# Optimization experiments

Measured on AMD Instinct MI355X. Metric: run time of the kernel, lower is better.

## Reference

```python
import jax, jax.numpy as jnp
from jax import lax
import numpy as np

D_MODEL = 1024
D_STATE = 64
D_CONV = 4
EXPAND = 2
HEADDIM = 64
D_INNER = EXPAND * D_MODEL          # 2048
NHEADS = D_INNER // HEADDIM         # 32
CHUNK = 64
CONV_DIM = D_INNER + 2 * D_STATE    # 2176
D_IN_PROJ = 2 * D_INNER + 2 * D_STATE + NHEADS  # 4256
B_SZ = 4
SEQLEN = 2048
EPS = 1e-5


def _silu(x):
    return x * jax.nn.sigmoid(x)


def _segsum(x):
    # x: [..., T]; returns [..., T, T] with [i,j] = sum_{j<k<=i} x[k], -inf above diag
    T = x.shape[-1]
    xe = jnp.broadcast_to(x[..., None], x.shape + (T,))
    strict_lower = jnp.tril(jnp.ones((T, T), bool), -1)
    xe = jnp.where(strict_lower, xe, 0.0)
    s = jnp.cumsum(xe, axis=-2)
    lower = jnp.tril(jnp.ones((T, T), bool), 0)
    return jnp.where(lower, s, -jnp.inf)


def setup_inputs() -> dict:
    key = jax.random.key(0)
    ks = jax.random.split(key, 5)
    u = jax.random.normal(ks[0], (B_SZ, SEQLEN, D_MODEL), jnp.float32)
    W_in = jax.random.normal(ks[1], (D_IN_PROJ, D_MODEL), jnp.float32) * 0.02
    conv_w = jax.random.normal(ks[2], (CONV_DIM, 1, D_CONV), jnp.float32) * 0.2  # depthwise kernel
    conv_b = jnp.zeros((CONV_DIM,), jnp.float32)
    dt_bias = jax.random.uniform(ks[3], (NHEADS,), jnp.float32, -1.0, 1.0)
    A_log = jnp.log(jnp.linspace(1.0, float(NHEADS), NHEADS)).astype(jnp.float32)
    D = jnp.ones((NHEADS,), jnp.float32)
    norm_w = jnp.ones((D_INNER,), jnp.float32)
    W_out = jax.random.normal(ks[4], (D_MODEL, D_INNER), jnp.float32) * 0.02
    return dict(u=u, W_in=W_in, conv_w=conv_w, conv_b=conv_b, dt_bias=dt_bias,
                A_log=A_log, D=D, norm_w=norm_w, W_out=W_out)


def reference(u, W_in, conv_w, conv_b, dt_bias, A_log, D, norm_w, W_out):
    b, s, _ = u.shape
    A = -jnp.exp(A_log)                                   # [H]
    zxbcdt = u @ W_in.T                                   # [b,s,D_IN_PROJ]
    z = zxbcdt[..., :D_INNER]
    xBC = zxbcdt[..., D_INNER:D_INNER + CONV_DIM]
    dt = jax.nn.softplus(zxbcdt[..., D_INNER + CONV_DIM:] + dt_bias)  # [b,s,H]

    # causal depthwise conv1d (left pad d_conv-1 == torch pad-both + slice[:s])
    xc = lax.conv_general_dilated(
        xBC.transpose(0, 2, 1), conv_w, window_strides=(1,),
        padding=[(D_CONV - 1, 0)], feature_group_count=CONV_DIM,
        dimension_numbers=('NCH', 'OIH', 'NCH'))
    xBC = _silu(xc.transpose(0, 2, 1) + conv_b)           # [b,s,CONV_DIM]

    x = xBC[..., :D_INNER].reshape(b, s, NHEADS, HEADDIM)
    Bm = xBC[..., D_INNER:D_INNER + D_STATE]              # [b,s,N]
    Cm = xBC[..., D_INNER + D_STATE:]                     # [b,s,N]

    # SSD chunked scan
    nch = s // CHUNK
    xs = (x * dt[..., None]).reshape(b, nch, CHUNK, NHEADS, HEADDIM)
    Ad = (A * dt).reshape(b, nch, CHUNK, NHEADS)
    Br = Bm.reshape(b, nch, CHUNK, D_STATE)
    Cr = Cm.reshape(b, nch, CHUNK, D_STATE)
    A_ch = Ad.transpose(0, 1, 3, 2)                       # [b,c,h,l]
    A_cum = jnp.cumsum(A_ch, axis=-1)
    L = jnp.exp(_segsum(A_ch))                            # [b,c,h,l,l]
    Y_diag = jnp.einsum('bcln,bcsn,bchls,bcshp->bclhp', Cr, Br, L, xs)
    decay_states = jnp.exp(A_cum[..., -1:] - A_cum)       # [b,c,h,l]
    states = jnp.einsum('bchl,bcln,bclhp->bchpn', decay_states, Br, xs)
    init = jnp.zeros((b, 1, NHEADS, HEADDIM, D_STATE), xs.dtype)
    states = jnp.concatenate([init, states], axis=1)      # [b,c+1,h,p,n]
    total_decay = jnp.pad(A_cum[..., -1].transpose(0, 2, 1), ((0, 0), (0, 0), (1, 0)))
    decay_chunk = jnp.exp(_segsum(total_decay))           # [b,h,c+1,c+1]
    new_states = jnp.einsum('bhzc,bchpn->bzhpn', decay_chunk, states)
    states = new_states[:, :-1]                           # [b,c,h,p,n]
    state_decay_out = jnp.exp(A_cum)
    Y_off = jnp.einsum('bcln,bchpn,bchl->bclhp', Cr, states, state_decay_out)
    y = (Y_diag + Y_off).reshape(b, s, NHEADS, HEADDIM)

    y = y + x * D[:, None]
    y = y.reshape(b, s, D_INNER)
    # gated RMSNorm
    y = y * _silu(z)
    y = y * lax.rsqrt(jnp.mean(y * y, axis=-1, keepdims=True) + EPS) * norm_w
    return y @ W_out.T
```

## Files before the change

### kernel.cpp

```cpp
#include <hip/hip_runtime.h>
#include <hip/hip_bf16.h>

#define BSZ 4
#define SEQ 2048
#define DMODEL 1024
#define DINNER 2048
#define DSTATE 64
#define NH 32
#define HD 64
#define CKL 64
#define NCH 32
#define CONVD 2176
#define DPROJ 4256
#define N1 4224
#define MTOT 8192
#define YSTR 72
#define CVTB 6272

typedef __hip_bfloat16 bf16;
typedef __attribute__((ext_vector_type(8))) short short8;
typedef __attribute__((ext_vector_type(4))) short short4_;
typedef __attribute__((ext_vector_type(4))) float f32x4;

__device__ __forceinline__ float sigmoidf_(float x) { return 1.0f / (1.0f + __expf(-x)); }
__device__ __forceinline__ float bits2f(short s) { return __uint_as_float(((unsigned)(unsigned short)s) << 16); }
__device__ __forceinline__ short f2bits(float f) {
    bf16 h = __float2bfloat16(f);
    return *reinterpret_cast<short*>(&h);
}

__device__ __forceinline__ void gl_lds16(const bf16* g, bf16* l) {
    __builtin_amdgcn_global_load_lds((const __attribute__((address_space(1))) void*)g,
                                     (__attribute__((address_space(3))) void*)l, 16, 0, 0);
}

__device__ __forceinline__ f32x4 MF(short8 a, short8 b, f32x4 c) {
    return __builtin_amdgcn_mfma_f32_16x16x32_bf16(a, b, c, 0, 0, 0);
}

template<int N> __device__ __forceinline__ void vmw() {
    if constexpr (N == 0)      asm volatile("s_waitcnt vmcnt(0)" ::: "memory");
    else if constexpr (N == 3) asm volatile("s_waitcnt vmcnt(3)" ::: "memory");
    else if constexpr (N == 6) asm volatile("s_waitcnt vmcnt(6)" ::: "memory");
    else                       asm volatile("s_waitcnt vmcnt(15)" ::: "memory");
}

__device__ __forceinline__ void swzx(int& bx, int& by) {
    int nx = gridDim.x;
    int nwg = nx * gridDim.y;
    int Lr = blockIdx.y * nx + blockIdx.x;
    int L = (Lr & 7) * (nwg >> 3) + (Lr >> 3);
    int GSZ = nx * 8;
    int g = L / GSZ, r = L - g * GSZ;
    bx = r % nx;
    by = g * 8 + r / nx;
}

__global__ __launch_bounds__(256) void k_pre2(const float* __restrict__ u, const float* __restrict__ W_in,
                                              const float* __restrict__ dt_bias,
                                              const float* __restrict__ W_out, const float* __restrict__ nw,
                                              bf16* __restrict__ u_b, float* __restrict__ dtt,
                                              bf16* __restrict__ win_b, bf16* __restrict__ wout_b) {
    __shared__ __align__(16) float us[8 * DMODEL];
    const int tid = threadIdx.x;
    if (blockIdx.x < CVTB) {
        int g = (blockIdx.x * 256 + tid) * 4;
        if (g < N1 * DMODEL) {
            f32x4 f = *(const f32x4*)&W_in[g];
            short4_ o;
#pragma unroll
            for (int j = 0; j < 4; j++) o[j] = f2bits(f[j]);
            *(short4_*)&win_b[g] = o;
        } else if (g < N1 * DMODEL + DMODEL * DINNER) {
            int g2 = g - N1 * DMODEL;
            f32x4 f = *(const f32x4*)&W_out[g2];
            f32x4 w = *(const f32x4*)&nw[g2 & (DINNER - 1)];
            short4_ o;
#pragma unroll
            for (int j = 0; j < 4; j++) o[j] = f2bits(f[j] * w[j]);
            *(short4_*)&wout_b[g2] = o;
        }
        return;
    }
    const int t0 = (blockIdx.x - CVTB) * 8;
    const float* ur = u + (size_t)t0 * DMODEL;
    bf16* ub = u_b + (size_t)t0 * DMODEL;
#pragma unroll
    for (int i = 0; i < 8; i++) {
        int idx = (i * 256 + tid) * 4;
        f32x4 v = *(const f32x4*)&ur[idx];
        *(f32x4*)&us[idx] = v;
        short4_ o;
#pragma unroll
        for (int j = 0; j < 4; j++) o[j] = f2bits(v[j]);
        *(short4_*)&ub[idx] = o;
    }
    __syncthreads();
    const int h = tid >> 3, sub = tid & 7;
    const float* wr = W_in + (size_t)(DPROJ - NH + h) * DMODEL;
    float s[8] = {};
    for (int k = sub * 4; k < DMODEL; k += 32) {
        f32x4 w4 = *(const f32x4*)&wr[k];
#pragma unroll
        for (int rr = 0; rr < 8; rr++) {
            f32x4 u4 = *(const f32x4*)&us[rr * DMODEL + k];
            s[rr] += u4[0] * w4[0] + u4[1] * w4[1] + u4[2] * w4[2] + u4[3] * w4[3];
        }
    }
#pragma unroll
    for (int rr = 0; rr < 8; rr++) {
        s[rr] += __shfl_down(s[rr], 4, 8);
        s[rr] += __shfl_down(s[rr], 2, 8);
        s[rr] += __shfl_down(s[rr], 1, 8);
    }
    if (sub == 0) {
        float bh = dt_bias[h];
#pragma unroll
        for (int rr = 0; rr < 8; rr++) {
            float x = s[rr] + bh;
            dtt[(size_t)h * MTOT + t0 + rr] = (x > 20.f) ? x : log1pf(__expf(x));
        }
    }
}

#define BARWAIT()                                           \
    __builtin_amdgcn_s_barrier();                           \
    asm volatile("s_waitcnt lgkmcnt(0)" ::: "memory");      \
    __builtin_amdgcn_sched_barrier(0);                      \
    __builtin_amdgcn_s_setprio(1)
#define ENDPH()                                             \
    __builtin_amdgcn_s_setprio(0);                          \
    __builtin_amdgcn_s_barrier()

__global__ __launch_bounds__(512, 2) void k_g1(const bf16* __restrict__ Ap,
                                               const bf16* __restrict__ Wp,
                                               bf16* __restrict__ Cp) {
    __shared__ __align__(16) short sA[2][16384];
    __shared__ __align__(16) short sB[2][12288];
    const int tid = threadIdx.x;
    const int lane = tid & 63, w = tid >> 6;
    const int wm = w >> 2, wn = w & 3;
    const int lr = lane & 15, lk = lane >> 4;
    int bx, by; swzx(bx, by);
    const int m0 = by * 256, n0 = bx * 192;
    const int ld = DMODEL;

    const int r8 = tid >> 3;
    const int c8 = ((tid & 7) ^ (r8 & 7)) * 8;
    const bf16* pA = Ap + (size_t)(m0 + r8) * ld + c8;
    const bf16* pB = Wp + (size_t)(n0 + r8) * ld + c8;

    auto stA = [&](int d, int t) {
#pragma unroll
        for (int h = 0; h < 2; h++)
#pragma unroll
            for (int q = 0; q < 2; q++)
                gl_lds16(pA + (size_t)(h * 128 + q * 64) * ld + t * 64,
                         (bf16*)&sA[d][h * 8192 + q * 4096 + tid * 8]);
    };
    auto stB = [&](int d, int u, int t) {
        gl_lds16(pB + (size_t)(u * 64) * ld + t * 64,
                 (bf16*)&sB[d][u * 4096 + tid * 8]);
    };

    const int c0 = (lk ^ (lr & 7)) * 8;
    const int c1 = ((lk + 4) ^ (lr & 7)) * 8;
    const int aR = (wm * 128 + lr) * 64;
    const int bR = (wn * 48 + lr) * 64;

    f32x4 acc[8][3];
#pragma unroll
    for (int i = 0; i < 8; i++)
#pragma unroll
        for (int j = 0; j < 3; j++) acc[i][j] = (f32x4){0.f, 0.f, 0.f, 0.f};
    short8 bfr[3][2], af[2][2];

#define RDA1(D, I)                                                   \
    af[0][0] = *(const short8*)&sA[D][aR + (I) * 1024 + c0];         \
    af[0][1] = *(const short8*)&sA[D][aR + (I) * 1024 + c1];         \
    af[1][0] = *(const short8*)&sA[D][aR + (I + 1) * 1024 + c0];     \
    af[1][1] = *(const short8*)&sA[D][aR + (I + 1) * 1024 + c1]
#define RDB1(D)                                                      \
    _Pragma("unroll")                                                \
    for (int jn = 0; jn < 3; ++jn) {                                 \
        bfr[jn][0] = *(const short8*)&sB[D][bR + jn * 1024 + c0];    \
        bfr[jn][1] = *(const short8*)&sB[D][bR + jn * 1024 + c1];    \
    }
#define MM1(I)                                                       \
    _Pragma("unroll")                                                \
    for (int hh = 0; hh < 2; ++hh) {                                 \
        _Pragma("unroll")                                            \
        for (int jn = 0; jn < 3; ++jn) {                             \
            acc[I][jn]     = MF(af[0][hh], bfr[jn][hh], acc[I][jn]); \
            acc[I + 1][jn] = MF(af[1][hh], bfr[jn][hh], acc[I + 1][jn]); \
        }                                                            \
    }

    stB(0, 0, 0); stB(0, 1, 0); stB(0, 2, 0); stA(0, 0);
    stB(1, 0, 1); stB(1, 1, 1); stB(1, 2, 1);
    vmw<3>();
    __builtin_amdgcn_s_barrier();

    for (int t0 = 0; t0 < 16; t0 += 2) {
        const int t1 = t0 + 1, t2 = t0 + 2, t3 = t0 + 3;
        const bool more = (t2 < 16);
        RDB1(0); RDA1(0, 0);
        stA(1, t1);
        BARWAIT(); MM1(0); ENDPH();
        RDA1(0, 2); if (more) stB(0, 0, t2);
        BARWAIT(); MM1(2); ENDPH();
        RDA1(0, 4); if (more) stB(0, 1, t2);
        BARWAIT(); MM1(4); ENDPH();
        RDA1(0, 6); if (more) stB(0, 2, t2);
        BARWAIT(); MM1(6);
        __builtin_amdgcn_s_setprio(0);
        if (more) vmw<3>(); else vmw<0>();
        __builtin_amdgcn_s_barrier();
        RDB1(1); RDA1(1, 0);
        if (more) stA(0, t2);
        BARWAIT(); MM1(0); ENDPH();
        RDA1(1, 2); if (more) stB(1, 0, t3);
        BARWAIT(); MM1(2); ENDPH();
        RDA1(1, 4); if (more) stB(1, 1, t3);
        BARWAIT(); MM1(4); ENDPH();
        RDA1(1, 6); if (more) stB(1, 2, t3);
        BARWAIT(); MM1(6);
        __builtin_amdgcn_s_setprio(0);
        if (more) vmw<3>();
        __builtin_amdgcn_s_barrier();
    }
#undef RDA1
#undef RDB1
#undef MM1

#pragma unroll
    for (int im = 0; im < 8; im++) {
        int row = m0 + wm * 128 + im * 16 + lk * 4;
#pragma unroll
        for (int jn = 0; jn < 3; jn++) {
            int col = n0 + wn * 48 + jn * 16 + lr;
            bf16* cp = Cp + (size_t)row * N1 + col;
#pragma unroll
            for (int rr = 0; rr < 4; rr++) cp[(size_t)rr * N1] = __float2bfloat16(acc[im][jn][rr]);
        }
    }
}

__global__ __launch_bounds__(512, 2) void k_g2(const bf16* __restrict__ Ap,
                                               const bf16* __restrict__ Wp,
                                               float* __restrict__ Cp) {
    __shared__ __align__(16) short sA[3][16384];
    __shared__ __align__(16) short sB[3][8192];
    __shared__ float rsrow[256];
    const int tid = threadIdx.x;
    const int lane = tid & 63, w = tid >> 6;
    const int wm = w >> 1, wn = w & 1;
    const int lr = lane & 15, lk = lane >> 4;
    int bx, by; swzx(bx, by);
    const int m0 = by * 256, n0 = bx * 128;
    const int lda = N1, ldb = DINNER;

    const int r8 = tid >> 3;
    const int c8 = ((tid & 7) ^ (r8 & 7)) * 8;
    const bf16* pA = Ap + (size_t)(m0 + r8) * lda + c8;
    const bf16* pB = Wp + (size_t)(n0 + r8) * ldb + c8;

    auto stA = [&](int d, int t) {
#pragma unroll
        for (int h = 0; h < 2; h++)
#pragma unroll
            for (int q = 0; q < 2; q++)
                gl_lds16(pA + (size_t)(h * 128 + q * 64) * lda + t * 64,
                         (bf16*)&sA[d][h * 8192 + q * 4096 + tid * 8]);
    };
    auto stB = [&](int d, int t) {
#pragma unroll
        for (int q = 0; q < 2; q++)
            gl_lds16(pB + (size_t)(q * 64) * ldb + t * 64,
                     (bf16*)&sB[d][q * 4096 + tid * 8]);
    };

    const int c0 = (lk ^ (lr & 7)) * 8;
    const int c1 = ((lk + 4) ^ (lr & 7)) * 8;
    const int aR = (wm * 64 + lr) * 64;
    const int bR = (wn * 64 + lr) * 64;

    f32x4 acc[4][4];
#pragma unroll
    for (int i = 0; i < 4; i++)
#pragma unroll
        for (int j = 0; j < 4; j++) acc[i][j] = (f32x4){0.f, 0.f, 0.f, 0.f};
    float ssq[4] = {0.f, 0.f, 0.f, 0.f};
    short8 bfr[4][2], af[2][2];

#define RDA2(D, I)                                                   \
    af[0][0] = *(const short8*)&sA[D][aR + (I) * 1024 + c0];         \
    af[0][1] = *(const short8*)&sA[D][aR + (I) * 1024 + c1];         \
    af[1][0] = *(const short8*)&sA[D][aR + (I + 1) * 1024 + c0];     \
    af[1][1] = *(const short8*)&sA[D][aR + (I + 1) * 1024 + c1]
#define RDB2(D)                                                      \
    _Pragma("unroll")                                                \
    for (int jn = 0; jn < 4; ++jn) {                                 \
        bfr[jn][0] = *(const short8*)&sB[D][bR + jn * 1024 + c0];    \
        bfr[jn][1] = *(const short8*)&sB[D][bR + jn * 1024 + c1];    \
    }
#define MM2(I)                                                       \
    _Pragma("unroll")                                                \
    for (int hh = 0; hh < 2; ++hh) {                                 \
        _Pragma("unroll")                                            \
        for (int jn = 0; jn < 4; ++jn) {                             \
            acc[I][jn]     = MF(af[0][hh], bfr[jn][hh], acc[I][jn]); \
            acc[I + 1][jn] = MF(af[1][hh], bfr[jn][hh], acc[I + 1][jn]); \
        }                                                            \
    }
#define SSQ2(I)                                                      \
    _Pragma("unroll")                                                \
    for (int hh = 0; hh < 2; ++hh)                                   \
        _Pragma("unroll")                                            \
        for (int e = 0; e < 8; ++e) {                                \
            float v0 = bits2f(af[0][hh][e]), v1 = bits2f(af[1][hh][e]); \
            ssq[I] += v0 * v0; ssq[I + 1] += v1 * v1;                \
        }

    stB(0, 0); stA(0, 0);
    stB(1, 1); stA(1, 1);
    vmw<6>();
    __builtin_amdgcn_s_barrier();

    int rb = 0, sb = 2;
    for (int t = 0; t < 32; ++t) {
        const bool more = (t + 2 < 32);
        RDB2(rb); RDA2(rb, 0);
        if (more) stB(sb, t + 2);
        BARWAIT(); MM2(0); SSQ2(0); ENDPH();
        RDA2(rb, 2);
        if (more) stA(sb, t + 2);
        BARWAIT(); MM2(2); SSQ2(2);
        __builtin_amdgcn_s_setprio(0);
        if (more) vmw<6>(); else if (t + 1 < 32) vmw<0>();
        __builtin_amdgcn_s_barrier();
        rb = (rb == 2) ? 0 : rb + 1;
        sb = (sb == 2) ? 0 : sb + 1;
    }
#undef RDA2
#undef RDB2
#undef MM2
#undef SSQ2

#pragma unroll
    for (int im = 0; im < 4; im++) {
        float s = ssq[im];
        s += __shfl_down(s, 32);
        s += __shfl_down(s, 16);
        if (lane < 16) rsrow[wm * 64 + im * 16 + lane] = rsqrtf(s * (1.0f / DINNER) + 1e-5f);
    }
    __syncthreads();
#pragma unroll
    for (int im = 0; im < 4; im++) {
        int rl = wm * 64 + im * 16 + lk * 4;
        int row = m0 + rl;
#pragma unroll
        for (int rr = 0; rr < 4; rr++) {
            float s = rsrow[rl + rr];
#pragma unroll
            for (int jn = 0; jn < 4; jn++) {
                int col = n0 + wn * 64 + jn * 16 + lr;
                Cp[(size_t)(row + rr) * DMODEL + col] = acc[im][jn][rr] * s;
            }
        }
    }
}

__global__ __launch_bounds__(256) void k_conv(const bf16* __restrict__ zx, const float* __restrict__ cw,
                                              const float* __restrict__ cb, bf16* __restrict__ xbc) {
    const int g = blockIdx.x * 256 + threadIdx.x;
    const int c0 = (g % 544) * 4;
    const int t0 = (g / 544) * 4;
    const int s0 = t0 & (SEQ - 1);
    const short* base = (const short*)(zx + (size_t)t0 * N1 + DINNER + c0);
    f32x4 w0 = *(const f32x4*)&cw[(c0 + 0) * 4];
    f32x4 w1 = *(const f32x4*)&cw[(c0 + 1) * 4];
    f32x4 w2 = *(const f32x4*)&cw[(c0 + 2) * 4];
    f32x4 w3 = *(const f32x4*)&cw[(c0 + 3) * 4];
    f32x4 bias = *(const f32x4*)&cb[c0];
    short4_ v[7];
#pragma unroll
    for (int o = 0; o < 7; o++) {
        if (s0 + o - 3 >= 0) v[o] = *(const short4_*)(base + (long)(o - 3) * N1);
        else v[o] = (short4_){0, 0, 0, 0};
    }
#pragma unroll
    for (int j = 0; j < 4; j++) {
        f32x4 a = bias;
#pragma unroll
        for (int k = 0; k < 4; k++) {
            short4_ x = v[j + k];
            a[0] += bits2f(x[0]) * w0[k];
            a[1] += bits2f(x[1]) * w1[k];
            a[2] += bits2f(x[2]) * w2[k];
            a[3] += bits2f(x[3]) * w3[k];
        }
        short4_ o_;
#pragma unroll
        for (int jj = 0; jj < 4; jj++) o_[jj] = f2bits(a[jj] * sigmoidf_(a[jj]));
        *(short4_*)((short*)xbc + (size_t)(t0 + j) * CONVD + c0) = o_;
    }
}

__global__ __launch_bounds__(256) void k_ssd(const bf16* __restrict__ xbc, const float* __restrict__ dtt,
                                             const float* __restrict__ A_log, const float* __restrict__ Dp,
                                             bf16* __restrict__ zx) {
    __shared__ __align__(16) short Ct[2][64 * YSTR];
    __shared__ __align__(16) short Bt[2][64 * YSTR];
    __shared__ __align__(16) short Bn[2][64 * YSTR];
    __shared__ __align__(16) short Xt[2][32 * YSTR];
    __shared__ __align__(16) short Sb[2][32 * YSTR];
    __shared__ __align__(16) short Gs[4 * 16 * YSTR];
    __shared__ __align__(16) float Sf[32 * 68];
    __shared__ __align__(16) float sdt2[2][64], sAc2[2][64], sf2[2][64];
    __shared__ float set2[2];

    const int ph = blockIdx.x, h = blockIdx.y, b = blockIdx.z;
    const int tid = threadIdx.x;
    const int lane = tid & 63, w = tid >> 6;
    const int lr = lane & 15, lk = lane >> 4;
    const float Ah = -__expf(A_log[h]);
    const float Dh = Dp[h];
    const int xcol = h * HD + ph * 32;

    const int lrow = tid >> 2, c0 = (tid & 3) * 16, px = (tid & 3) * 8;
    const int zl = 16 * w + (lane >> 2), zp = (lane & 3) * 8;

    short8 rC0, rC1, rB0, rB1, rX, rZ;
    float rdt;
    auto load_chunk = [&](int cc) {
        int rows0 = b * SEQ + cc * CKL;
        const short* rp = (const short*)(xbc + (size_t)(rows0 + lrow) * CONVD);
        rC0 = *(const short8*)&rp[DINNER + DSTATE + c0];
        rC1 = *(const short8*)&rp[DINNER + DSTATE + c0 + 8];
        rB0 = *(const short8*)&rp[DINNER + c0];
        rB1 = *(const short8*)&rp[DINNER + c0 + 8];
        rX  = *(const short8*)&rp[xcol + px];
        rZ  = *(const short8*)((const short*)zx + (size_t)(rows0 + zl) * N1 + xcol + zp);
        rdt = dtt[(size_t)h * MTOT + rows0 + lane];
    };
    auto scatter = [&](int buf) {
        *(short8*)&Ct[buf][lrow * YSTR + c0] = rC0;
        *(short8*)&Ct[buf][lrow * YSTR + c0 + 8] = rC1;
        *(short8*)&Bt[buf][lrow * YSTR + c0] = rB0;
        *(short8*)&Bt[buf][lrow * YSTR + c0 + 8] = rB1;
#pragma unroll
        for (int j = 0; j < 8; j++) {
            Bn[buf][(c0 + j) * YSTR + lrow] = rB0[j];
            Bn[buf][(c0 + 8 + j) * YSTR + lrow] = rB1[j];
            Xt[buf][(px + j) * YSTR + lrow] = rX[j];
        }
    };
    auto dtscan = [&](int buf) {
        if (tid < 64) {
            float dv = rdt;
            float v = Ah * dv;
#pragma unroll
            for (int d = 1; d < 64; d <<= 1) { float o = __shfl_up(v, d); if (tid >= d) v += o; }
            float tot = __shfl(v, 63);
            sdt2[buf][tid] = dv; sAc2[buf][tid] = v; sf2[buf][tid] = __expf(tot - v) * dv;
            if (tid == 63) set2[buf] = __expf(tot);
        }
    };

    for (int i = tid; i < 32 * 68; i += 256) Sf[i] = 0.f;
    for (int i = tid; i < 32 * YSTR; i += 256) Sb[0][i] = 0;
    load_chunk(0);
    scatter(0);
    dtscan(0);
    __syncthreads();

    for (int c = 0; c < NCH; c++) {
        const int par = c & 1, nb = par ^ 1;
        const int rows0 = b * SEQ + c * CKL;
        float etot = set2[par];
        short8 zcur = rZ;
        if (c + 1 < NCH) load_chunk(c + 1);

        short8 cf0 = *(const short8*)&Ct[par][(16 * w + lr) * YSTR + lk * 8];
        short8 cf1 = *(const short8*)&Ct[par][(16 * w + lr) * YSTR + 32 + lk * 8];
        f32x4 acc[2];
#pragma unroll
        for (int t = 0; t < 2; t++) {
            short8 s0 = *(const short8*)&Sb[par][(16 * t + lr) * YSTR + lk * 8];
            short8 s1 = *(const short8*)&Sb[par][(16 * t + lr) * YSTR + 32 + lk * 8];
            acc[t] = MF(cf0, s0, (f32x4){0.f, 0.f, 0.f, 0.f});
            acc[t] = MF(cf1, s1, acc[t]);
        }
        float sAcl[4], el[4];
#pragma unroll
        for (int rr = 0; rr < 4; rr++) { sAcl[rr] = sAc2[par][16 * w + lk * 4 + rr]; el[rr] = __expf(sAcl[rr]); }
#pragma unroll
        for (int t = 0; t < 2; t++)
#pragma unroll
            for (int rr = 0; rr < 4; rr++) acc[t][rr] *= el[rr];
        short* gw = Gs + w * 16 * YSTR;
#pragma unroll
        for (int t = 0; t < 4; t++) {
            short8 b0 = *(const short8*)&Bt[par][(16 * t + lr) * YSTR + lk * 8];
            short8 b1 = *(const short8*)&Bt[par][(16 * t + lr) * YSTR + 32 + lk * 8];
            f32x4 g = MF(cf0, b0, (f32x4){0.f, 0.f, 0.f, 0.f});
            g = MF(cf1, b1, g);
            int s = 16 * t + lr;
            float sAcs = sAc2[par][s], dts = sdt2[par][s];
#pragma unroll
            for (int rr = 0; rr < 4; rr++) {
                int l = 16 * w + lk * 4 + rr;
                float v = (s <= l) ? g[rr] * __expf(sAcl[rr] - sAcs) * dts : 0.f;
                gw[(lk * 4 + rr) * YSTR + s] = f2bits(v);
            }
        }
        short8 gf0 = *(const short8*)&gw[lr * YSTR + lk * 8];
        short8 gf1 = *(const short8*)&gw[lr * YSTR + 32 + lk * 8];
#pragma unroll
        for (int t = 0; t < 2; t++) {
            short8 x0 = *(const short8*)&Xt[par][(16 * t + lr) * YSTR + lk * 8];
            short8 x1 = *(const short8*)&Xt[par][(16 * t + lr) * YSTR + 32 + lk * 8];
            acc[t] = MF(gf0, x0, acc[t]);
            acc[t] = MF(gf1, x1, acc[t]);
        }
        {
            int pw = w & 1, nh2 = w >> 1;
            short8 xt0 = *(const short8*)&Xt[par][(16 * pw + lr) * YSTR + lk * 8];
            short8 xt1 = *(const short8*)&Xt[par][(16 * pw + lr) * YSTR + 32 + lk * 8];
            f32x4 sa0 = *(const f32x4*)&sf2[par][lk * 8];
            f32x4 sa1 = *(const f32x4*)&sf2[par][lk * 8 + 4];
            f32x4 sb0 = *(const f32x4*)&sf2[par][32 + lk * 8];
            f32x4 sb1 = *(const f32x4*)&sf2[par][32 + lk * 8 + 4];
            short8 xd0, xd1;
#pragma unroll
            for (int j = 0; j < 4; j++) {
                xd0[j]     = f2bits(bits2f(xt0[j])     * sa0[j]);
                xd0[4 + j] = f2bits(bits2f(xt0[4 + j]) * sa1[j]);
                xd1[j]     = f2bits(bits2f(xt1[j])     * sb0[j]);
                xd1[4 + j] = f2bits(bits2f(xt1[4 + j]) * sb1[j]);
            }
#pragma unroll
            for (int j = 0; j < 2; j++) {
                int nt = 2 * nh2 + j;
                short8 b0 = *(const short8*)&Bn[par][(16 * nt + lr) * YSTR + lk * 8];
                short8 b1 = *(const short8*)&Bn[par][(16 * nt + lr) * YSTR + 32 + lk * 8];
                f32x4 sacc = MF(xd0, b0, (f32x4){0.f, 0.f, 0.f, 0.f});
                sacc = MF(xd1, b1, sacc);
#pragma unroll
                for (int rr = 0; rr < 4; rr++) {
                    int n = 16 * nt + lr;
                    int p = 16 * pw + lk * 4 + rr;
                    float nv = Sf[p * 68 + n] * etot + sacc[rr];
                    Sf[p * 68 + n] = nv;
                    Sb[nb][p * YSTR + n] = f2bits(nv);
                }
            }
        }
#pragma unroll
        for (int t = 0; t < 2; t++) {
#pragma unroll
            for (int rr = 0; rr < 4; rr++) {
                int p = 16 * t + lr;
                int l = 16 * w + lk * 4 + rr;
                float y = acc[t][rr] + Dh * bits2f(Xt[par][p * YSTR + l]);
                Ct[par][l * YSTR + p] = f2bits(y);
            }
        }
        {
            short8 y8 = *(const short8*)&Ct[par][zl * YSTR + zp];
            short* zpp = (short*)zx + (size_t)(rows0 + zl) * N1 + xcol + zp;
            short8 o;
#pragma unroll
            for (int j = 0; j < 8; j++) {
                float z = bits2f(zcur[j]);
                o[j] = f2bits(bits2f(y8[j]) * (z * sigmoidf_(z)));
            }
            *(short8*)zpp = o;
        }
        if (c + 1 < NCH) {
            scatter(nb);
            dtscan(nb);
        }
        __syncthreads();
    }
}

extern "C" void kernel_launch(void* const* d_in, const int* in_sizes, int n_in,
                              void* d_out, int out_size, void* d_ws, size_t ws_size,
                              hipStream_t stream) {
    const float* u       = (const float*)d_in[0];
    const float* W_in    = (const float*)d_in[1];
    const float* conv_w  = (const float*)d_in[2];
    const float* conv_b  = (const float*)d_in[3];
    const float* dt_bias = (const float*)d_in[4];
    const float* A_log   = (const float*)d_in[5];
    const float* Dp      = (const float*)d_in[6];
    const float* norm_w  = (const float*)d_in[7];
    const float* W_out   = (const float*)d_in[8];
    float* out = (float*)d_out;

    char* ws = (char*)d_ws;
    bf16* zx     = (bf16*)ws;  ws += (size_t)MTOT * N1 * 2;
    bf16* xbc    = (bf16*)ws;  ws += (size_t)MTOT * CONVD * 2;
    bf16* wout_b = (bf16*)ws;  ws += (size_t)DMODEL * DINNER * 2;
    float* dtt   = (float*)ws; ws += (size_t)NH * MTOT * 4;

    bf16* u_b   = (bf16*)d_out;
    bf16* win_b = (bf16*)((char*)d_out + (size_t)MTOT * DMODEL * 2);

    k_pre2<<<CVTB + MTOT / 8, 256, 0, stream>>>(u, W_in, dt_bias, W_out, norm_w,
                                                u_b, dtt, win_b, wout_b);

    k_g1<<<dim3(N1 / 192, MTOT / 256), 512, 0, stream>>>(u_b, win_b, zx);

    k_conv<<<(MTOT / 4) * (CONVD / 4) / 256, 256, 0, stream>>>(zx, conv_w, conv_b, xbc);

    k_ssd<<<dim3(2, NH, BSZ), 256, 0, stream>>>(xbc, dtt, A_log, Dp, zx);

    k_g2<<<dim3(DMODEL / 128, MTOT / 256), 512, 0, stream>>>(zx, wout_b, out);
}
```

Before: 374.4 us.

## Precompute dt cumsum/decay in separate kernel and fold decay into B scatter

Moves the per-chunk dt prefix scan, decay factors and chunk total decay out of the serial SSD loop into a small new kernel that writes them to workspace. The state-update decay factor is now multiplied into B during the transposed LDS scatter, so the per-iteration scaling of X before the state MFMA is dropped. The transposed Bn/Xt LDS tiles get a wider stride with a per-row offset to reduce bank conflicts. This adds an extra launch and extra global reads and writes of scan results, and changes where the bf16 rounding happens.

```diff
diff --git a/kernel.cpp b/kernel.cpp
--- a/kernel.cpp
+++ b/kernel.cpp
@@ -15,6 +15,7 @@
 #define N1 4224
 #define MTOT 8192
 #define YSTR 72
+#define YSTR2 120
 #define CVTB 6272
 
 typedef __hip_bfloat16 bf16;
@@ -120,6 +121,27 @@
             float x = s[rr] + bh;
             dtt[(size_t)h * MTOT + t0 + rr] = (x > 20.f) ? x : log1pf(__expf(x));
         }
+    }
+}
+
+__global__ __launch_bounds__(256) void k_dts(const float* __restrict__ dtt, const float* __restrict__ A_log,
+                                             float* __restrict__ sAc, float* __restrict__ sfv,
+                                             float* __restrict__ etot) {
+    const int h = blockIdx.x, b = blockIdx.y;
+    const int tid = threadIdx.x, w = tid >> 6, lane = tid & 63;
+    const float Ah = -__expf(A_log[h]);
+#pragma unroll
+    for (int g = 0; g < 8; g++) {
+        int c = g * 4 + w;
+        int t0 = b * SEQ + c * CKL;
+        float dv = dtt[(size_t)h * MTOT + t0 + lane];
+        float v = Ah * dv;
+#pragma unroll
+        for (int d = 1; d < 64; d <<= 1) { float o = __shfl_up(v, d); if (lane >= d) v += o; }
+        float tot = __shfl(v, 63);
+        sAc[(size_t)h * MTOT + t0 + lane] = v;
+        sfv[(size_t)h * MTOT + t0 + lane] = __expf(tot - v) * dv;
+        if (lane == 63) etot[(h * BSZ + b) * NCH + c] = __expf(tot);
     }
 }
 
@@ -408,23 +430,23 @@
 }
 
 __global__ __launch_bounds__(256) void k_ssd(const bf16* __restrict__ xbc, const float* __restrict__ dtt,
-                                             const float* __restrict__ A_log, const float* __restrict__ Dp,
+                                             const float* __restrict__ sAc, const float* __restrict__ sfv,
+                                             const float* __restrict__ etg, const float* __restrict__ Dp,
                                              bf16* __restrict__ zx) {
     __shared__ __align__(16) short Ct[2][64 * YSTR];
     __shared__ __align__(16) short Bt[2][64 * YSTR];
-    __shared__ __align__(16) short Bn[2][64 * YSTR];
-    __shared__ __align__(16) short Xt[2][32 * YSTR];
+    __shared__ __align__(16) short Bn[2][64 * YSTR2];
+    __shared__ __align__(16) short Xt[2][32 * YSTR2];
     __shared__ __align__(16) short Sb[2][32 * YSTR];
     __shared__ __align__(16) short Gs[4 * 16 * YSTR];
     __shared__ __align__(16) float Sf[32 * 68];
-    __shared__ __align__(16) float sdt2[2][64], sAc2[2][64], sf2[2][64];
-    __shared__ float set2[2];
+    __shared__ __align__(16) float sdt2[2][64], sAc2[2][64];
+    __shared__ float etl[NCH];
 
     const int ph = blockIdx.x, h = blockIdx.y, b = blockIdx.z;
     const int tid = threadIdx.x;
     const int lane = tid & 63, w = tid >> 6;
     const int lr = lane & 15, lk = lane >> 4;
-    const float Ah = -__expf(A_log[h]);
     const float Dh = Dp[h];
     const int xcol = h * HD + ph * 32;
 
@@ -432,7 +454,7 @@
     const int zl = 16 * w + (lane >> 2), zp = (lane & 3) * 8;
 
     short8 rC0, rC1, rB0, rB1, rX, rZ;
-    float rdt;
+    float rdt, rsa, rsf;
     auto load_chunk = [&](int cc) {
         int rows0 = b * SEQ + cc * CKL;
         const short* rp = (const short*)(xbc + (size_t)(rows0 + lrow) * CONVD);
@@ -443,6 +465,8 @@
         rX  = *(const short8*)&rp[xcol + px];
         rZ  = *(const short8*)((const short*)zx + (size_t)(rows0 + zl) * N1 + xcol + zp);
         rdt = dtt[(size_t)h * MTOT + rows0 + lane];
+        rsa = sAc[(size_t)h * MTOT + rows0 + lane];
+        rsf = sfv[(size_t)h * MTOT + rows0 + lrow];
     };
     auto scatter = [&](int buf) {
         *(short8*)&Ct[buf][lrow * YSTR + c0] = rC0;
@@ -451,34 +475,25 @@
         *(short8*)&Bt[buf][lrow * YSTR + c0 + 8] = rB1;
 #pragma unroll
         for (int j = 0; j < 8; j++) {
-            Bn[buf][(c0 + j) * YSTR + lrow] = rB0[j];
-            Bn[buf][(c0 + 8 + j) * YSTR + lrow] = rB1[j];
-            Xt[buf][(px + j) * YSTR + lrow] = rX[j];
-        }
-    };
-    auto dtscan = [&](int buf) {
-        if (tid < 64) {
-            float dv = rdt;
-            float v = Ah * dv;
-#pragma unroll
-            for (int d = 1; d < 64; d <<= 1) { float o = __shfl_up(v, d); if (tid >= d) v += o; }
-            float tot = __shfl(v, 63);
-            sdt2[buf][tid] = dv; sAc2[buf][tid] = v; sf2[buf][tid] = __expf(tot - v) * dv;
-            if (tid == 63) set2[buf] = __expf(tot);
-        }
+            int n0_ = c0 + j, n1_ = c0 + 8 + j, p_ = px + j;
+            Bn[buf][n0_ * YSTR2 + lrow + (n0_ >> 3) * 8] = f2bits(bits2f(rB0[j]) * rsf);
+            Bn[buf][n1_ * YSTR2 + lrow + (n1_ >> 3) * 8] = f2bits(bits2f(rB1[j]) * rsf);
+            Xt[buf][p_ * YSTR2 + lrow + (p_ >> 3) * 8] = rX[j];
+        }
+        if (tid < 64) { sdt2[buf][tid] = rdt; sAc2[buf][tid] = rsa; }
     };
 
     for (int i = tid; i < 32 * 68; i += 256) Sf[i] = 0.f;
     for (int i = tid; i < 32 * YSTR; i += 256) Sb[0][i] = 0;
+    if (tid < NCH) etl[tid] = etg[(h * BSZ + b) * NCH + tid];
     load_chunk(0);
     scatter(0);
-    dtscan(0);
     __syncthreads();
 
     for (int c = 0; c < NCH; c++) {
         const int par = c & 1, nb = par ^ 1;
         const int rows0 = b * SEQ + c * CKL;
-        float etot = set2[par];
+        float etot = etl[c];
         short8 zcur = rZ;
         if (c + 1 < NCH) load_chunk(c + 1);
 
@@ -519,34 +534,25 @@
         short8 gf1 = *(const short8*)&gw[lr * YSTR + 32 + lk * 8];
 #pragma unroll
         for (int t = 0; t < 2; t++) {
-            short8 x0 = *(const short8*)&Xt[par][(16 * t + lr) * YSTR + lk * 8];
-            short8 x1 = *(const short8*)&Xt[par][(16 * t + lr) * YSTR + 32 + lk * 8];
+            int xr = 16 * t + lr;
+            short8 x0 = *(const short8*)&Xt[par][xr * YSTR2 + ((xr >> 3) + lk) * 8];
+            short8 x1 = *(const short8*)&Xt[par][xr * YSTR2 + 32 + ((xr >> 3) + lk) * 8];
             acc[t] = MF(gf0, x0, acc[t]);
             acc[t] = MF(gf1, x1, acc[t]);
         }
         {
             int pw = w & 1, nh2 = w >> 1;
-            short8 xt0 = *(const short8*)&Xt[par][(16 * pw + lr) * YSTR + lk * 8];
-            short8 xt1 = *(const short8*)&Xt[par][(16 * pw + lr) * YSTR + 32 + lk * 8];
-            f32x4 sa0 = *(const f32x4*)&sf2[par][lk * 8];
-            f32x4 sa1 = *(const f32x4*)&sf2[par][lk * 8 + 4];
-            f32x4 sb0 = *(const f32x4*)&sf2[par][32 + lk * 8];
-            f32x4 sb1 = *(const f32x4*)&sf2[par][32 + lk * 8 + 4];
-            short8 xd0, xd1;
-#pragma unroll
-            for (int j = 0; j < 4; j++) {
-                xd0[j]     = f2bits(bits2f(xt0[j])     * sa0[j]);
-                xd0[4 + j] = f2bits(bits2f(xt0[4 + j]) * sa1[j]);
-                xd1[j]     = f2bits(bits2f(xt1[j])     * sb0[j]);
-                xd1[4 + j] = f2bits(bits2f(xt1[4 + j]) * sb1[j]);
-            }
+            const int xp = 16 * pw + lr;
+            short8 xt0 = *(const short8*)&Xt[par][xp * YSTR2 + ((xp >> 3) + lk) * 8];
+            short8 xt1 = *(const short8*)&Xt[par][xp * YSTR2 + 32 + ((xp >> 3) + lk) * 8];
 #pragma unroll
             for (int j = 0; j < 2; j++) {
                 int nt = 2 * nh2 + j;
-                short8 b0 = *(const short8*)&Bn[par][(16 * nt + lr) * YSTR + lk * 8];
-                short8 b1 = *(const short8*)&Bn[par][(16 * nt + lr) * YSTR + 32 + lk * 8];
-                f32x4 sacc = MF(xd0, b0, (f32x4){0.f, 0.f, 0.f, 0.f});
-                sacc = MF(xd1, b1, sacc);
+                int nr = 16 * nt + lr;
+                short8 b0 = *(const short8*)&Bn[par][nr * YSTR2 + ((nr >> 3) + lk) * 8];
+                short8 b1 = *(const short8*)&Bn[par][nr * YSTR2 + 32 + ((nr >> 3) + lk) * 8];
+                f32x4 sacc = MF(xt0, b0, (f32x4){0.f, 0.f, 0.f, 0.f});
+                sacc = MF(xt1, b1, sacc);
 #pragma unroll
                 for (int rr = 0; rr < 4; rr++) {
                     int n = 16 * nt + lr;
@@ -563,7 +569,7 @@
             for (int rr = 0; rr < 4; rr++) {
                 int p = 16 * t + lr;
                 int l = 16 * w + lk * 4 + rr;
-                float y = acc[t][rr] + Dh * bits2f(Xt[par][p * YSTR + l]);
+                float y = acc[t][rr] + Dh * bits2f(Xt[par][p * YSTR2 + l + (p >> 3) * 8]);
                 Ct[par][l * YSTR + p] = f2bits(y);
             }
         }
@@ -580,7 +586,6 @@
         }
         if (c + 1 < NCH) {
             scatter(nb);
-            dtscan(nb);
         }
         __syncthreads();
     }
@@ -605,18 +610,22 @@
     bf16* xbc    = (bf16*)ws;  ws += (size_t)MTOT * CONVD * 2;
     bf16* wout_b = (bf16*)ws;  ws += (size_t)DMODEL * DINNER * 2;
     float* dtt   = (float*)ws; ws += (size_t)NH * MTOT * 4;
+    float* sAcw  = (float*)ws; ws += (size_t)NH * MTOT * 4;
+    float* sfvw  = (float*)ws; ws += (size_t)NH * MTOT * 4;
+    float* etotw = (float*)ws; ws += 64 * 1024;
 
     bf16* u_b   = (bf16*)d_out;
     bf16* win_b = (bf16*)((char*)d_out + (size_t)MTOT * DMODEL * 2);
 
     k_pre2<<<CVTB + MTOT / 8, 256, 0, stream>>>(u, W_in, dt_bias, W_out, norm_w,
                                                 u_b, dtt, win_b, wout_b);
+    k_dts<<<dim3(NH, BSZ), 256, 0, stream>>>(dtt, A_log, sAcw, sfvw, etotw);
 
     k_g1<<<dim3(N1 / 192, MTOT / 256), 512, 0, stream>>>(u_b, win_b, zx);
 
     k_conv<<<(MTOT / 4) * (CONVD / 4) / 256, 256, 0, stream>>>(zx, conv_w, conv_b, xbc);
 
-    k_ssd<<<dim3(2, NH, BSZ), 256, 0, stream>>>(xbc, dtt, A_log, Dp, zx);
+    k_ssd<<<dim3(2, NH, BSZ), 256, 0, stream>>>(xbc, dtt, sAcw, sfvw, etotw, Dp, zx);
 
     k_g2<<<dim3(DMODEL / 128, MTOT / 256), 512, 0, stream>>>(zx, wout_b, out);
 }
```

Measured after the change: 376.7 us. No clear change (+0.6%).
